# Kernel tuning notes

Measured on AMD Instinct MI355X. Metric: run time of the kernel, lower is better.

Reference implementation:

```python
import jax, jax.numpy as jnp
import numpy as np

WS = 8  # window size

def _rel_pos_index(ws):
    coords = np.stack(np.meshgrid(np.arange(ws), np.arange(ws), indexing='ij'))  # (2,ws,ws)
    cf = coords.reshape(2, -1)
    rel = (cf[:, :, None] - cf[:, None, :]).transpose(1, 2, 0).astype(np.int64)
    rel[..., 0] += ws - 1
    rel[..., 1] += ws - 1
    rel[..., 0] *= 2 * ws - 1
    return rel.sum(-1)  # (ws*ws, ws*ws)

REL_IDX = jnp.asarray(_rel_pos_index(WS).reshape(-1))

def _layernorm(x, g, b, eps=1e-5):
    m = x.mean(-1, keepdims=True)
    v = x.var(-1, keepdims=True)
    return (x - m) / jnp.sqrt(v + eps) * g + b

def setup_inputs() -> dict:
    key = jax.random.key(0)
    ks = jax.random.split(key, 32)
    B, Cw, Cs, H, W = 8, 64, 64, 128, 128
    dim, nH, hid = 256, 8, 1024
    n_bias = (2 * WS - 1) * (2 * WS - 1)
    s = 0.02
    d = {}
    d['LH'] = jax.random.normal(ks[0], (B, Cw, H, W), jnp.float32)
    d['HL'] = jax.random.normal(ks[1], (B, Cw, H, W), jnp.float32)
    d['HH'] = jax.random.normal(ks[2], (B, Cw, H, W), jnp.float32)
    d['Spat'] = jax.random.normal(ks[3], (B, Cs, H, W), jnp.float32)
    d['w_hllh'] = jax.random.normal(ks[4], (dim, 2 * Cw), jnp.float32) * s
    d['b_hllh'] = jnp.zeros((dim,), jnp.float32)
    d['w_hh'] = jax.random.normal(ks[5], (dim, Cw), jnp.float32) * s
    d['b_hh'] = jnp.zeros((dim,), jnp.float32)
    d['w_spat'] = jax.random.normal(ks[6], (dim, Cs), jnp.float32) * s
    d['b_spat'] = jnp.zeros((dim,), jnp.float32)
    d['ln1x_g'] = jnp.ones((dim,), jnp.float32)
    d['ln1x_b'] = jnp.zeros((dim,), jnp.float32)
    d['ln1y_g'] = jnp.ones((dim,), jnp.float32)
    d['ln1y_b'] = jnp.zeros((dim,), jnp.float32)
    d['qkv_w'] = jax.random.normal(ks[7], (dim, dim), jnp.float32) * s
    d['qkv_b'] = jnp.zeros((dim,), jnp.float32)
    d['qkv2_w'] = jax.random.normal(ks[8], (dim, dim), jnp.float32) * s
    d['qkv2_b'] = jnp.zeros((dim,), jnp.float32)
    d['qkv3_w'] = jax.random.normal(ks[9], (dim, dim), jnp.float32) * s
    d['qkv3_b'] = jnp.zeros((dim,), jnp.float32)
    d['proj_w'] = jax.random.normal(ks[10], (dim, dim), jnp.float32) * s
    d['proj_b'] = jnp.zeros((dim,), jnp.float32)
    d['rpb_table'] = jax.random.normal(ks[11], (n_bias, nH), jnp.float32) * s
    d['ln2_g'] = jnp.ones((dim,), jnp.float32)
    d['ln2_b'] = jnp.zeros((dim,), jnp.float32)
    d['fc1_w'] = jax.random.normal(ks[12], (hid, dim), jnp.float32) * s
    d['fc1_b'] = jnp.zeros((hid,), jnp.float32)
    d['fc2_w'] = jax.random.normal(ks[13], (dim, hid), jnp.float32) * s
    d['fc2_b'] = jnp.zeros((dim,), jnp.float32)
    return d

def _fwd(LH, HL, HH, Spat, w_hllh, b_hllh, w_hh, b_hh, w_spat, b_spat,
         ln1x_g, ln1x_b, ln1y_g, ln1y_b, qkv_w, qkv_b, qkv2_w, qkv2_b,
         qkv3_w, qkv3_b, proj_w, proj_b, rpb_table, ln2_g, ln2_b,
         fc1_w, fc1_b, fc2_w, fc2_b):
    B, _, H, W = LH.shape
    C = w_hllh.shape[0]
    nH = rpb_table.shape[1]
    hd = C // nH
    N = WS * WS
    # 1x1 convs to common dim, NHWC
    x = jnp.einsum('bchw,oc->bhwo', jnp.concatenate([LH, HL], axis=1), w_hllh) + b_hllh
    z0 = jnp.einsum('bchw,oc->bhwo', HH, w_hh) + b_hh
    y = jnp.einsum('bchw,oc->bhwo', Spat, w_spat) + b_spat
    shortcut = z0.reshape(B, H * W, C)
    xn = _layernorm(x, ln1x_g, ln1x_b)
    yn = _layernorm(y, ln1y_g, ln1y_b)
    # window partition (H,W divisible by WS)
    def part(t):
        t = t.reshape(B, H // WS, WS, W // WS, WS, C).transpose(0, 1, 3, 2, 4, 5)
        return t.reshape(-1, N, C)
    xw = part(xn)
    yw = part(yn)
    zw = yw  # original code: z = F.pad(y, ...) -> value stream is normalized y
    def heads(t, Wm, bm):
        return (t @ Wm.T + bm).reshape(-1, N, nH, hd).transpose(0, 2, 1, 3)
    q = heads(xw, qkv_w, qkv_b) * (hd ** -0.5)
    k = heads(yw, qkv2_w, qkv2_b)
    v = heads(zw, qkv3_w, qkv3_b)
    attn = jnp.einsum('bhnd,bhmd->bhnm', q, k)
    rpb = rpb_table[REL_IDX].reshape(N, N, nH).transpose(2, 0, 1)  # (nH,N,N)
    attn = jax.nn.softmax(attn + rpb[None], axis=-1)
    out = jnp.einsum('bhnm,bhmd->bnhd', attn, v).reshape(-1, N, C)
    out = out @ proj_w.T + proj_b
    # window reverse
    out = out.reshape(B, H // WS, W // WS, WS, WS, C).transpose(0, 1, 3, 2, 4, 5).reshape(B, H * W, C)
    zt = shortcut + out
    h = _layernorm(zt, ln2_g, ln2_b)
    h = jax.nn.gelu(h @ fc1_w.T + fc1_b, approximate=False) @ fc2_w.T + fc2_b
    zt = zt + h
    return zt.reshape(B, H, W, C).transpose(0, 3, 1, 2)

def reference(LH, HL, HH, Spat, w_hllh, b_hllh, w_hh, b_hh, w_spat, b_spat,
              ln1x_g, ln1x_b, ln1y_g, ln1y_b, qkv_w, qkv_b, qkv2_w, qkv2_b,
              qkv3_w, qkv3_b, proj_w, proj_b, rpb_table, ln2_g, ln2_b,
              fc1_w, fc1_b, fc2_w, fc2_b):
    return _fwd(LH, HL, HH, Spat, w_hllh, b_hllh, w_hh, b_hh, w_spat, b_spat,
                ln1x_g, ln1x_b, ln1y_g, ln1y_b, qkv_w, qkv_b, qkv2_w, qkv2_b,
                qkv3_w, qkv3_b, proj_w, proj_b, rpb_table, ln2_g, ln2_b,
                fc1_w, fc1_b, fc2_w, fc2_b)
```

## Files before the change

### kernel.cpp

```cpp
#include <hip/hip_runtime.h>
#include <math.h>

#define DI static __device__ __forceinline__

typedef __attribute__((ext_vector_type(8))) short bhalf8;
typedef __attribute__((ext_vector_type(4))) float floatx4;

DI unsigned short f2bf(float f){
  union { float f; unsigned u; } v; v.f = f;
  unsigned r = (v.u + 0x7fffu + ((v.u >> 16) & 1u)) >> 16;
  return (unsigned short)r;
}
DI float bflo(unsigned v){ return __uint_as_float(v << 16); }
DI float bfhi(unsigned v){ return __uint_as_float(v & 0xffff0000u); }
DI unsigned pk2(float a, float b){ return (unsigned)f2bf(a) | ((unsigned)f2bf(b) << 16); }
DI void unpack8(uint4 u, float* a){
  a[0]=bflo(u.x); a[1]=bfhi(u.x); a[2]=bflo(u.y); a[3]=bfhi(u.y);
  a[4]=bflo(u.z); a[5]=bfhi(u.z); a[6]=bflo(u.w); a[7]=bfhi(u.w);
}
DI float fc(float4 v, int j){ return j==0 ? v.x : (j==1 ? v.y : (j==2 ? v.z : v.w)); }
DI float gelu(float x){
  float u = x*(0.7978845608f + 0.0356774081f*x*x);
  float e = __expf(2.f*u);
  return x - x/(e + 1.f);
}

__global__ void k_scale_vec(const float* __restrict__ src, float* __restrict__ dst, int n, float s){
  int i = blockIdx.x*256 + threadIdx.x;
  if (i < n) dst[i] = src[i]*s;
}
__global__ void k_fragw(const float* __restrict__ src, unsigned short* __restrict__ dst,
                        int n, int K, float scale){
  int t = blockIdx.x*256 + threadIdx.x;
  if (t >= n) return;
  int j = t & 7, lane = (t >> 3) & 63, rest = t >> 9;
  int KS = K >> 5;
  int ks = rest % KS, nt = rest / KS;
  int row = nt*16 + (lane & 15);
  int col = ks*32 + ((lane >> 4) << 3) + j;
  dst[t] = f2bf(src[(size_t)row*K + col] * scale);
}
__global__ void k_bias(const float* __restrict__ rpb, float* __restrict__ biasf){
  int t = blockIdx.x*256 + threadIdx.x;
  int r = t & 3, lane = (t>>2) & 63, nt = (t>>8) & 3, mt = (t>>10) & 3, h = t>>12;
  int qtok = mt*16 + (lane>>4)*4 + r;
  int ktok = nt*16 + (lane & 15);
  int idx = ((qtok>>3) - (ktok>>3) + 7)*15 + ((qtok&7) - (ktok&7) + 7);
  biasf[t] = rpb[idx*8 + h];
}

__global__ __launch_bounds__(256) void k_front(
    const float* __restrict__ LH, const float* __restrict__ HL,
    const float* __restrict__ HH, const float* __restrict__ Sp,
    const unsigned short* __restrict__ wxf, const float* __restrict__ bx,
    const unsigned short* __restrict__ wzf, const float* __restrict__ bz,
    const unsigned short* __restrict__ wyf, const float* __restrict__ by,
    const float* __restrict__ g1x, const float* __restrict__ b1x,
    const float* __restrict__ g1y, const float* __restrict__ b1y,
    const unsigned short* __restrict__ wqf, const float* __restrict__ bq,
    const unsigned short* __restrict__ wkf, const float* __restrict__ bk,
    const unsigned short* __restrict__ wvf, const float* __restrict__ bv,
    unsigned short* __restrict__ z0, unsigned short* __restrict__ qg,
    unsigned short* __restrict__ kg, unsigned short* __restrict__ vtg)
{
  __shared__ __align__(16) unsigned short astg[64*72];
  __shared__ __align__(16) unsigned short sbufA[64*288];
  __shared__ __align__(16) unsigned short sbufB[64*264];
  float* part  = (float*)(sbufA + 16896);
  float* stats = part + 512;

  const int tid = threadIdx.x;
  const int lane = tid & 63, wave = tid >> 6, col = lane & 15, quad = lane >> 4;
  const int mB = blockIdx.x << 6;
  const int b  = mB >> 14;
  const int p0 = mB & 16383;
  const int hrow = p0 >> 7, w0 = p0 & 127;
  const int winb = b*256 + (hrow>>3)*16 + (w0>>3);
  const int tokrow = (hrow & 7)*8;
  const size_t pbase = (size_t)b * (64*16384) + p0;

  float4 f0, f1, f2, f3;
  auto stage_load = [&](const float* plane){
    const float* src = plane + (size_t)((tid>>4)*4)*16384 + (tid&15)*4;
    f0 = *(const float4*)(src);
    f1 = *(const float4*)(src + 16384);
    f2 = *(const float4*)(src + 32768);
    f3 = *(const float4*)(src + 49152);
  };
  auto stage_store = [&](){
    const int tq = tid & 15, c4 = (tid >> 4) * 4;
    #pragma unroll
    for (int j=0;j<4;++j){
      int tok = tq*4 + j;
      int kk = c4 ^ (((tok>>1)&7)<<3);
      uint2 u;
      u.x = pk2(fc(f0,j), fc(f1,j));
      u.y = pk2(fc(f2,j), fc(f3,j));
      *(uint2*)(astg + tok*72 + kk) = u;
    }
  };

  floatx4 c[4][4];
  auto zeroc = [&](){
    #pragma unroll
    for (int mt=0;mt<4;++mt)
      #pragma unroll
      for (int nt=0;nt<4;++nt) c[mt][nt] = (floatx4){0.f,0.f,0.f,0.f};
  };
  auto conv_step = [&](const unsigned short* wf, int KS, int ksg0){
    #pragma unroll
    for (int ksl=0; ksl<2; ++ksl){
      bhalf8 a[4];
      #pragma unroll
      for (int mt=0;mt<4;++mt){
        int tok = mt*16 + col;
        int kk = (ksl*32 + (quad<<3)) ^ (((tok>>1)&7)<<3);
        a[mt] = *(const bhalf8*)(astg + tok*72 + kk);
      }
      #pragma unroll
      for (int nt=0;nt<4;++nt){
        bhalf8 bfr = *(const bhalf8*)(wf + (size_t)(((wave*4+nt)*KS + ksg0 + ksl)*64 + lane)*8);
        #pragma unroll
        for (int mt=0;mt<4;++mt)
          c[mt][nt] = __builtin_amdgcn_mfma_f32_16x16x32_bf16(a[mt], bfr, c[mt][nt], 0, 0, 0);
      }
    }
  };
  auto ln_frag = [&](const float* bias, const float* g, const float* bb2, unsigned short* dst){
    float bv[4];
    #pragma unroll
    for (int nt=0;nt<4;++nt) bv[nt] = bias[wave*64 + nt*16 + col];
    #pragma unroll
    for (int mt=0;mt<4;++mt){
      #pragma unroll
      for (int r=0;r<4;++r){
        float s=0.f, q=0.f;
        #pragma unroll
        for (int nt=0;nt<4;++nt){
          float v = c[mt][nt][r] + bv[nt];
          c[mt][nt][r] = v; s += v; q += v*v;
        }
        s += __shfl_xor(s,1); q += __shfl_xor(q,1);
        s += __shfl_xor(s,2); q += __shfl_xor(q,2);
        s += __shfl_xor(s,4); q += __shfl_xor(q,4);
        s += __shfl_xor(s,8); q += __shfl_xor(q,8);
        if (col == 0){
          int tok = mt*16 + quad*4 + r;
          part[(wave*64+tok)*2+0] = s;
          part[(wave*64+tok)*2+1] = q;
        }
      }
    }
    __syncthreads();
    if (tid < 64){
      float s=0.f, q=0.f;
      #pragma unroll
      for (int w2=0;w2<4;++w2){ s += part[(w2*64+tid)*2]; q += part[(w2*64+tid)*2+1]; }
      float mean = s*(1.f/256.f);
      float var  = q*(1.f/256.f) - mean*mean;
      stats[tid*2]   = mean;
      stats[tid*2+1] = rsqrtf(var + 1e-5f);
    }
    __syncthreads();
    float gv[4], av[4];
    #pragma unroll
    for (int nt=0;nt<4;++nt){ int ch = wave*64+nt*16+col; gv[nt] = g[ch]; av[nt] = bb2[ch]; }
    #pragma unroll
    for (int mt=0;mt<4;++mt)
      #pragma unroll
      for (int r=0;r<4;++r){
        int tok = mt*16 + quad*4 + r;
        float mean = stats[tok*2], rstd = stats[tok*2+1];
        #pragma unroll
        for (int nt=0;nt<4;++nt)
          dst[tok*264 + wave*64 + nt*16 + col] = f2bf((c[mt][nt][r]-mean)*rstd*gv[nt] + av[nt]);
      }
    __syncthreads();
  };

  auto gemm = [&](const unsigned short* Abuf, const unsigned short* wf, const float* bias){
    #pragma unroll
    for (int mt=0;mt<4;++mt)
      #pragma unroll
      for (int nt=0;nt<4;++nt) c[mt][nt] = (floatx4){0.f,0.f,0.f,0.f};
    #pragma unroll
    for (int ks=0; ks<8; ++ks){
      bhalf8 a[4];
      #pragma unroll
      for (int mt=0;mt<4;++mt)
        a[mt] = *(const bhalf8*)(Abuf + (mt*16+col)*264 + ks*32 + (quad<<3));
      #pragma unroll
      for (int nt=0;nt<4;++nt){
        bhalf8 bf = *(const bhalf8*)(wf + (size_t)(((wave*4+nt)*8 + ks)*64 + lane)*8);
        #pragma unroll
        for (int mt=0;mt<4;++mt)
          c[mt][nt] = __builtin_amdgcn_mfma_f32_16x16x32_bf16(a[mt], bf, c[mt][nt], 0, 0, 0);
      }
    }
    #pragma unroll
    for (int nt=0;nt<4;++nt){
      float bb2 = bias[wave*64 + nt*16 + col];
      #pragma unroll
      for (int mt=0;mt<4;++mt)
        #pragma unroll
        for (int r=0;r<4;++r) c[mt][nt][r] += bb2;
    }
  };
  auto stage_write = [&](unsigned short* gout){
    __syncthreads();
    #pragma unroll
    for (int mt=0;mt<4;++mt)
      #pragma unroll
      for (int nt=0;nt<4;++nt)
        #pragma unroll
        for (int r=0;r<4;++r)
          sbufA[(mt*16+quad*4+r)*264 + wave*64 + nt*16 + col] = f2bf(c[mt][nt][r]);
    __syncthreads();
    int tok = tid >> 2, c0 = (tid & 3)*64;
    const uint4* s = (const uint4*)(sbufA + tok*264 + c0);
    uint4* d = (uint4*)(gout + ((size_t)(winb + (tok>>3)))*16384
                             + (size_t)(tokrow + (tok&7))*256 + c0);
    #pragma unroll
    for (int i=0;i<8;++i) d[i] = s[i];
  };

  stage_load(HH + pbase);
  stage_store();
  __syncthreads();
  stage_load(LH + pbase);
  zeroc(); conv_step(wzf, 2, 0);
  {
    #pragma unroll
    for (int nt=0;nt<4;++nt){
      float bzv = bz[wave*64 + nt*16 + col];
      #pragma unroll
      for (int mt=0;mt<4;++mt)
        #pragma unroll
        for (int r=0;r<4;++r) c[mt][nt][r] += bzv;
    }
  }
  stage_write(z0);
  stage_store();
  __syncthreads();
  stage_load(HL + pbase);
  zeroc(); conv_step(wxf, 4, 0);
  __syncthreads();
  stage_store();
  __syncthreads();
  stage_load(Sp + pbase);
  conv_step(wxf, 4, 2);
  __syncthreads();
  stage_store();
  ln_frag(bx, g1x, b1x, sbufA);
  zeroc(); conv_step(wyf, 2, 0);
  ln_frag(by, g1y, b1y, sbufB);
  gemm(sbufA, wqf, bq);
  stage_write(qg);
  gemm(sbufB, wkf, bk);
  stage_write(kg);
  gemm(sbufB, wvf, bv);
  __syncthreads();
  #pragma unroll
  for (int mt=0;mt<4;++mt)
    #pragma unroll
    for (int nt=0;nt<4;++nt){
      int ch = wave*64 + nt*16 + col;
      uint2 u; u.x = pk2(c[mt][nt][0], c[mt][nt][1]); u.y = pk2(c[mt][nt][2], c[mt][nt][3]);
      *(uint2*)(sbufA + ch*72 + mt*16 + quad*4) = u;
    }
  __syncthreads();
  {
    int ch = tid;
    #pragma unroll
    for (int wi=0; wi<8; ++wi){
      uint4 val = *(const uint4*)(sbufA + ch*72 + wi*8);
      *(uint4*)(vtg + ((size_t)(winb + wi))*16384 + ch*64 + tokrow) = val;
    }
  }
}

__global__ __launch_bounds__(256, 2) void k_attnproj(
    const unsigned short* __restrict__ qg, const unsigned short* kg,
    const unsigned short* vtg, const float* __restrict__ biasf,
    const unsigned short* __restrict__ wpf, const float* __restrict__ bp,
    const unsigned short* __restrict__ z0, unsigned short* kvz)
{
  __shared__ __align__(16) unsigned short Pb[4*64*72];
  __shared__ __align__(16) unsigned short Ob[64*264];
  const int tid = threadIdx.x, lane = tid & 63, wave = tid >> 6;
  const int col = lane & 15, quad = lane >> 4;
  const int win = blockIdx.x;
  const size_t wbase = (size_t)win * 16384;
  const unsigned short* qw = qg + wbase;
  const unsigned short* kw = kg + wbase;
  const unsigned short* vw = vtg + wbase;
  unsigned short* Pw = Pb + wave*64*72;

  #pragma unroll 1
  for (int hh=0; hh<2; ++hh){
    const int h = wave*2 + hh;
    bhalf8 qf[4], kf[4];
    #pragma unroll
    for (int mt=0;mt<4;++mt)
      qf[mt] = *(const bhalf8*)(qw + (mt*16+col)*256 + h*32 + (quad<<3));
    #pragma unroll
    for (int nt=0;nt<4;++nt)
      kf[nt] = *(const bhalf8*)(kw + (nt*16+col)*256 + h*32 + (quad<<3));
    floatx4 S[4][4];
    #pragma unroll
    for (int mt=0;mt<4;++mt)
      #pragma unroll
      for (int nt=0;nt<4;++nt) S[mt][nt] = (floatx4){0.f,0.f,0.f,0.f};
    #pragma unroll
    for (int mt=0;mt<4;++mt)
      #pragma unroll
      for (int nt=0;nt<4;++nt)
        S[mt][nt] = __builtin_amdgcn_mfma_f32_16x16x32_bf16(qf[mt], kf[nt], S[mt][nt], 0, 0, 0);
    #pragma unroll
    for (int mt=0;mt<4;++mt)
      #pragma unroll
      for (int nt=0;nt<4;++nt){
        float4 bb = *(const float4*)(biasf + (size_t)(((h*4+mt)*4+nt))*256 + lane*4);
        S[mt][nt][0] += bb.x; S[mt][nt][1] += bb.y; S[mt][nt][2] += bb.z; S[mt][nt][3] += bb.w;
      }
    float linv[4][4];
    #pragma unroll
    for (int mt=0;mt<4;++mt){
      #pragma unroll
      for (int r=0;r<4;++r){
        float mx = fmaxf(fmaxf(S[mt][0][r], S[mt][1][r]), fmaxf(S[mt][2][r], S[mt][3][r]));
        mx = fmaxf(mx, __shfl_xor(mx, 1));
        mx = fmaxf(mx, __shfl_xor(mx, 2));
        mx = fmaxf(mx, __shfl_xor(mx, 4));
        mx = fmaxf(mx, __shfl_xor(mx, 8));
        float e0 = __expf(S[mt][0][r]-mx), e1 = __expf(S[mt][1][r]-mx);
        float e2 = __expf(S[mt][2][r]-mx), e3 = __expf(S[mt][3][r]-mx);
        S[mt][0][r]=e0; S[mt][1][r]=e1; S[mt][2][r]=e2; S[mt][3][r]=e3;
        float l = e0+e1+e2+e3;
        l += __shfl_xor(l, 1);
        l += __shfl_xor(l, 2);
        l += __shfl_xor(l, 4);
        l += __shfl_xor(l, 8);
        linv[mt][r] = 1.f/l;
      }
    }
    #pragma unroll
    for (int mt=0;mt<4;++mt)
      #pragma unroll
      for (int nt=0;nt<4;++nt)
        #pragma unroll
        for (int r=0;r<4;++r)
          Pw[(mt*16+quad*4+r)*72 + nt*16 + col] = f2bf(S[mt][nt][r]);
    asm volatile("s_waitcnt lgkmcnt(0)" ::: "memory");
    floatx4 O[4][2];
    #pragma unroll
    for (int mt=0;mt<4;++mt){ O[mt][0]=(floatx4){0.f,0.f,0.f,0.f}; O[mt][1]=(floatx4){0.f,0.f,0.f,0.f}; }
    #pragma unroll
    for (int ks=0; ks<2; ++ks){
      bhalf8 vf[2];
      #pragma unroll
      for (int nt2=0;nt2<2;++nt2)
        vf[nt2] = *(const bhalf8*)(vw + (h*32 + nt2*16 + col)*64 + ks*32 + (quad<<3));
      #pragma unroll
      for (int mt=0;mt<4;++mt){
        bhalf8 pf = *(const bhalf8*)(Pw + (mt*16+col)*72 + ks*32 + (quad<<3));
        #pragma unroll
        for (int nt2=0;nt2<2;++nt2)
          O[mt][nt2] = __builtin_amdgcn_mfma_f32_16x16x32_bf16(pf, vf[nt2], O[mt][nt2], 0, 0, 0);
      }
    }
    #pragma unroll
    for (int mt=0;mt<4;++mt)
      #pragma unroll
      for (int nt2=0;nt2<2;++nt2)
        #pragma unroll
        for (int r=0;r<4;++r)
          Ob[(mt*16+quad*4+r)*264 + h*32 + nt2*16 + col] = f2bf(O[mt][nt2][r]*linv[mt][r]);
  }
  __syncthreads();

  floatx4 c[4][4];
  #pragma unroll
  for (int mt=0;mt<4;++mt)
    #pragma unroll
    for (int nt=0;nt<4;++nt) c[mt][nt] = (floatx4){0.f,0.f,0.f,0.f};
  #pragma unroll
  for (int ks=0; ks<8; ++ks){
    bhalf8 a[4];
    #pragma unroll
    for (int mt=0;mt<4;++mt)
      a[mt] = *(const bhalf8*)(Ob + (mt*16+col)*264 + ks*32 + (quad<<3));
    #pragma unroll
    for (int nt=0;nt<4;++nt){
      bhalf8 bf = *(const bhalf8*)(wpf + (size_t)(((wave*4+nt)*8 + ks)*64 + lane)*8);
      #pragma unroll
      for (int mt=0;mt<4;++mt)
        c[mt][nt] = __builtin_amdgcn_mfma_f32_16x16x32_bf16(a[mt], bf, c[mt][nt], 0, 0, 0);
    }
  }
  float bb[4];
  #pragma unroll
  for (int nt=0;nt<4;++nt) bb[nt] = bp[wave*64 + nt*16 + col];

  float* obuf = (float*)Pb;
  unsigned short* ztb = kvz + (size_t)win * 16384;
  #pragma unroll
  for (int p=0; p<2; ++p){
    __syncthreads();
    #pragma unroll
    for (int mt2=0;mt2<2;++mt2){
      int mt = p*2 + mt2;
      #pragma unroll
      for (int nt=0;nt<4;++nt)
        #pragma unroll
        for (int r=0;r<4;++r)
          obuf[(mt2*16+quad*4+r)*260 + wave*64 + nt*16 + col] = c[mt][nt][r] + bb[nt];
    }
    __syncthreads();
    {
      int tl = tid >> 3, c0 = (tid & 7)*32;
      int tok = p*32 + tl;
      const float4* s = (const float4*)(obuf + tl*260 + c0);
      const uint4* zp = (const uint4*)(z0 + ((size_t)win*64 + tok)*256 + c0);
      float zv[32];
      #pragma unroll
      for (int i=0;i<4;++i) unpack8(zp[i], zv + i*8);
      uint4* d = (uint4*)(ztb + (size_t)tok*256 + c0);
      #pragma unroll
      for (int i=0;i<4;++i){
        float4 a = s[2*i], b4 = s[2*i+1];
        float r0 = a.x  + zv[i*8+0], r1 = a.y  + zv[i*8+1];
        float r2 = a.z  + zv[i*8+2], r3 = a.w  + zv[i*8+3];
        float r4 = b4.x + zv[i*8+4], r5 = b4.y + zv[i*8+5];
        float r6 = b4.z + zv[i*8+6], r7 = b4.w + zv[i*8+7];
        uint4 u;
        u.x = pk2(r0,r1); u.y = pk2(r2,r3); u.z = pk2(r4,r5); u.w = pk2(r6,r7);
        d[i] = u;
      }
    }
  }
}

__global__ __launch_bounds__(256, 2) void k_mlp(
    const unsigned short* __restrict__ kvzt,
    const float* __restrict__ g2, const float* __restrict__ b2,
    const unsigned short* __restrict__ w1f, const float* __restrict__ fc1b,
    const unsigned short* __restrict__ w2f, const float* __restrict__ fc2b,
    float* __restrict__ out)
{
  __shared__ __align__(16) unsigned short smu[2*64*264];
  unsigned short* ztn  = smu;
  unsigned short* hbuf = smu + 64*264;
  float* ob = (float*)smu;

  const int tid  = threadIdx.x;
  const int mB   = blockIdx.x << 6;
  const int lane = tid & 63, wave = tid >> 6;
  const int col  = lane & 15, quad = lane >> 4;

  const int bb_ = mB >> 14;
  const int pp0 = mB & 16383;
  const int hrow = pp0 >> 7, w0 = pp0 & 127;
  const int winb = bb_*256 + (hrow>>3)*16 + (w0>>3);
  const int tokrow = (hrow & 7)*8;
  auto ztrow = [&](int tok)->size_t{
    return ((size_t)(winb + (tok>>3))*64 + (size_t)(tokrow + (tok&7))) * 256;
  };

  {
    const int tok = tid >> 2, qd = tid & 3;
    const uint4* zr = (const uint4*)(kvzt + ztrow(tok) + qd*64);
    float v[64];
    #pragma unroll
    for (int j=0;j<8;++j) unpack8(zr[j], v + j*8);
    float s=0.f, q=0.f;
    #pragma unroll
    for (int j=0;j<64;++j){ s += v[j]; q += v[j]*v[j]; }
    s += __shfl_xor(s,1); q += __shfl_xor(q,1);
    s += __shfl_xor(s,2); q += __shfl_xor(q,2);
    float mean = s*(1.f/256.f);
    float rstd = rsqrtf(q*(1.f/256.f) - mean*mean + 1e-5f);
    unsigned short* zd = ztn + tok*264 + qd*64;
    const float4* gp = (const float4*)(g2 + qd*64);
    const float4* bp = (const float4*)(b2 + qd*64);
    #pragma unroll
    for (int j8=0;j8<8;++j8){
      float4 g0 = gp[j8*2], g1 = gp[j8*2+1];
      float4 u0 = bp[j8*2], u1 = bp[j8*2+1];
      float r0 = (v[j8*8+0]-mean)*rstd*g0.x + u0.x;
      float r1 = (v[j8*8+1]-mean)*rstd*g0.y + u0.y;
      float r2 = (v[j8*8+2]-mean)*rstd*g0.z + u0.z;
      float r3 = (v[j8*8+3]-mean)*rstd*g0.w + u0.w;
      float r4 = (v[j8*8+4]-mean)*rstd*g1.x + u1.x;
      float r5 = (v[j8*8+5]-mean)*rstd*g1.y + u1.y;
      float r6 = (v[j8*8+6]-mean)*rstd*g1.z + u1.z;
      float r7 = (v[j8*8+7]-mean)*rstd*g1.w + u1.w;
      uint4 u;
      u.x=pk2(r0,r1); u.y=pk2(r2,r3); u.z=pk2(r4,r5); u.w=pk2(r6,r7);
      *(uint4*)(zd + j8*8) = u;
    }
  }
  __syncthreads();

  floatx4 oacc[4][4];
  #pragma unroll
  for (int i=0;i<4;++i)
    #pragma unroll
    for (int j=0;j<4;++j) oacc[i][j] = (floatx4){0.f,0.f,0.f,0.f};

  #pragma unroll 1
  for (int hb=0; hb<4; ++hb){
    float bv1[4];
    #pragma unroll
    for (int nt=0;nt<4;++nt) bv1[nt] = fc1b[hb*256 + wave*64 + nt*16 + col];
    #pragma unroll 1
    for (int mt=0; mt<4; ++mt){
      floatx4 hacc[4];
      #pragma unroll
      for (int nt=0;nt<4;++nt) hacc[nt] = (floatx4){0.f,0.f,0.f,0.f};
      #pragma unroll
      for (int ks=0; ks<8; ++ks){
        bhalf8 a = *(const bhalf8*)(ztn + (mt*16 + col)*264 + ks*32 + (quad<<3));
        #pragma unroll
        for (int nt=0; nt<4; ++nt){
          int gnt = hb*16 + wave*4 + nt;
          bhalf8 b = *(const bhalf8*)(w1f + (size_t)((gnt*8 + ks)*64 + lane)*8);
          hacc[nt] = __builtin_amdgcn_mfma_f32_16x16x32_bf16(a, b, hacc[nt], 0, 0, 0);
        }
      }
      #pragma unroll
      for (int nt=0; nt<4; ++nt){
        int ch = wave*64 + nt*16 + col;
        #pragma unroll
        for (int r=0;r<4;++r)
          hbuf[(mt*16 + quad*4 + r)*264 + ch] = f2bf(gelu(hacc[nt][r] + bv1[nt]));
      }
    }
    __syncthreads();
    #pragma unroll
    for (int mt=0; mt<4; ++mt){
      #pragma unroll
      for (int ks=0; ks<8; ++ks){
        bhalf8 a = *(const bhalf8*)(hbuf + (mt*16 + col)*264 + ks*32 + (quad<<3));
        #pragma unroll
        for (int ot=0; ot<4; ++ot){
          int go = wave*4 + ot;
          bhalf8 b = *(const bhalf8*)(w2f + (size_t)((go*32 + hb*8 + ks)*64 + lane)*8);
          oacc[mt][ot] = __builtin_amdgcn_mfma_f32_16x16x32_bf16(a, b, oacc[mt][ot], 0, 0, 0);
        }
      }
    }
    __syncthreads();
  }

  #pragma unroll
  for (int ot=0; ot<4; ++ot){
    int o = wave*64 + ot*16 + col;
    float bo = fc2b[o];
    #pragma unroll
    for (int mt=0; mt<4; ++mt){
      #pragma unroll
      for (int r=0;r<4;++r){
        int tok = mt*16 + quad*4 + r;
        float zv = bflo((unsigned)kvzt[ztrow(tok) + o]);
        ob[tok*257 + o] = oacc[mt][ot][r] + bo + zv;
      }
    }
  }
  __syncthreads();
  {
    const int b = mB >> 14, hw0 = mB & 16383;
    float* obase = out + (size_t)b*(256*16384) + hw0;
    #pragma unroll 1
    for (int it=0; it<64; ++it){
      int l = it*256 + tid;
      int o = l >> 6, tk = l & 63;
      obase[(size_t)o*16384 + tk] = ob[tk*257 + o];
    }
  }
}

extern "C" void kernel_launch(void* const* d_in, const int* in_sizes, int n_in,
                              void* d_out, int out_size, void* d_ws, size_t ws_size,
                              hipStream_t stream)
{
  (void)in_sizes; (void)n_in; (void)out_size; (void)ws_size;
  const float* LH    = (const float*)d_in[0];
  const float* HL    = (const float*)d_in[1];
  const float* HH    = (const float*)d_in[2];
  const float* Spat  = (const float*)d_in[3];
  const float* w_hllh= (const float*)d_in[4];
  const float* b_hllh= (const float*)d_in[5];
  const float* w_hh  = (const float*)d_in[6];
  const float* b_hh  = (const float*)d_in[7];
  const float* w_spat= (const float*)d_in[8];
  const float* b_spat= (const float*)d_in[9];
  const float* ln1x_g= (const float*)d_in[10];
  const float* ln1x_b= (const float*)d_in[11];
  const float* ln1y_g= (const float*)d_in[12];
  const float* ln1y_b= (const float*)d_in[13];
  const float* qkv_w = (const float*)d_in[14];
  const float* qkv_b = (const float*)d_in[15];
  const float* qkv2_w= (const float*)d_in[16];
  const float* qkv2_b= (const float*)d_in[17];
  const float* qkv3_w= (const float*)d_in[18];
  const float* qkv3_b= (const float*)d_in[19];
  const float* proj_w= (const float*)d_in[20];
  const float* proj_b= (const float*)d_in[21];
  const float* rpb   = (const float*)d_in[22];
  const float* ln2_g = (const float*)d_in[23];
  const float* ln2_b = (const float*)d_in[24];
  const float* fc1_w = (const float*)d_in[25];
  const float* fc1_b = (const float*)d_in[26];
  const float* fc2_w = (const float*)d_in[27];
  const float* fc2_b = (const float*)d_in[28];
  float* out = (float*)d_out;

  char* ws = (char*)d_ws;
  size_t off = 0;
  auto alloc = [&](size_t bytes)->void*{
    void* p = ws + off; off += (bytes + 255) & ~(size_t)255; return p;
  };
  const size_t M = 131072;
  unsigned short* z0  = (unsigned short*)alloc(M*256*2);
  unsigned short* qg  = (unsigned short*)alloc(M*256*2);
  char* kv_region     = (char*)alloc(M*256*4);
  unsigned short* kg  = (unsigned short*)kv_region;
  unsigned short* vtg = (unsigned short*)(kv_region + M*256*2);
  unsigned short* ztb = (unsigned short*)kv_region;
  unsigned short* wxf = (unsigned short*)alloc(256*128*2);
  unsigned short* wzf = (unsigned short*)alloc(256*64*2);
  unsigned short* wyf = (unsigned short*)alloc(256*64*2);
  unsigned short* wqf = (unsigned short*)alloc(256*256*2);
  unsigned short* wkf = (unsigned short*)alloc(256*256*2);
  unsigned short* wvf = (unsigned short*)alloc(256*256*2);
  unsigned short* wpf = (unsigned short*)alloc(256*256*2);
  unsigned short* w1f = (unsigned short*)alloc(1024*256*2);
  unsigned short* w2f = (unsigned short*)alloc(256*1024*2);
  float* biasf = (float*)alloc(32768*4);
  float* bqs = (float*)alloc(256*4);

  const float sc = 0.17677669529663687f;
  k_fragw<<<dim3(128),  dim3(256), 0, stream>>>(w_hllh, wxf, 256*128, 128, 1.f);
  k_fragw<<<dim3(64),   dim3(256), 0, stream>>>(w_hh,   wzf, 256*64,  64,  1.f);
  k_fragw<<<dim3(64),   dim3(256), 0, stream>>>(w_spat, wyf, 256*64,  64,  1.f);
  k_fragw<<<dim3(256),  dim3(256), 0, stream>>>(qkv_w,  wqf, 256*256, 256, sc);
  k_fragw<<<dim3(256),  dim3(256), 0, stream>>>(qkv2_w, wkf, 256*256, 256, 1.f);
  k_fragw<<<dim3(256),  dim3(256), 0, stream>>>(qkv3_w, wvf, 256*256, 256, 1.f);
  k_fragw<<<dim3(256),  dim3(256), 0, stream>>>(proj_w, wpf, 256*256, 256, 1.f);
  k_fragw<<<dim3(1024), dim3(256), 0, stream>>>(fc1_w,  w1f, 1024*256, 256, 1.f);
  k_fragw<<<dim3(1024), dim3(256), 0, stream>>>(fc2_w,  w2f, 256*1024, 1024, 1.f);
  k_bias <<<dim3(128),  dim3(256), 0, stream>>>(rpb, biasf);
  k_scale_vec<<<dim3(1), dim3(256), 0, stream>>>(qkv_b, bqs, 256, sc);

  k_front<<<dim3(2048), dim3(256), 0, stream>>>(LH, HL, HH, Spat,
      wxf, b_hllh, wzf, b_hh, wyf, b_spat,
      ln1x_g, ln1x_b, ln1y_g, ln1y_b,
      wqf, bqs, wkf, qkv2_b, wvf, qkv3_b,
      z0, qg, kg, vtg);
  k_attnproj<<<dim3(2048), dim3(256), 0, stream>>>(qg, kg, vtg, biasf, wpf, proj_b, z0, ztb);
  k_mlp<<<dim3(2048), dim3(256), 0, stream>>>(ztb, ln2_g, ln2_b,
      w1f, fc1_b, w2f, fc2_b, out);
}
```

Measured before the change: 810.4 us.

## Merge weight prep launches, reorder fragment layout, vectorize output stores

Eleven small preprocessing kernels are combined into one k_prep launch that dispatches on block index, which removes per-launch overhead. The weight fragment layout becomes lane-major with the k-step index innermost, so each lane's consecutive k-steps sit contiguously, and every GEMM's B-fragment addressing is updated to match. The final NCHW output store now writes float2 pairs, halving the store instruction count. The layout change could weaken coalescing across lanes within one load, since neighbouring lanes are now KS*16 bytes apart.

```diff
diff --git a/kernel.cpp b/kernel.cpp
--- a/kernel.cpp
+++ b/kernel.cpp
@@ -25,28 +25,62 @@
   return x - x/(e + 1.f);
 }
 
-__global__ void k_scale_vec(const float* __restrict__ src, float* __restrict__ dst, int n, float s){
-  int i = blockIdx.x*256 + threadIdx.x;
-  if (i < n) dst[i] = src[i]*s;
-}
-__global__ void k_fragw(const float* __restrict__ src, unsigned short* __restrict__ dst,
-                        int n, int K, float scale){
-  int t = blockIdx.x*256 + threadIdx.x;
-  if (t >= n) return;
-  int j = t & 7, lane = (t >> 3) & 63, rest = t >> 9;
-  int KS = K >> 5;
-  int ks = rest % KS, nt = rest / KS;
+DI void frag_pack(const float* __restrict__ src, unsigned short* __restrict__ dst,
+                  int t, int K, int ksbits, float scale){
+  int j = t & 7;
+  int ks = (t >> 3) & ((1<<ksbits)-1);
+  int lane = (t >> (3+ksbits)) & 63;
+  int nt = t >> (9+ksbits);
   int row = nt*16 + (lane & 15);
-  int col = ks*32 + ((lane >> 4) << 3) + j;
+  int col = (ks<<5) + ((lane >> 4) << 3) + j;
   dst[t] = f2bf(src[(size_t)row*K + col] * scale);
 }
-__global__ void k_bias(const float* __restrict__ rpb, float* __restrict__ biasf){
-  int t = blockIdx.x*256 + threadIdx.x;
-  int r = t & 3, lane = (t>>2) & 63, nt = (t>>8) & 3, mt = (t>>10) & 3, h = t>>12;
-  int qtok = mt*16 + (lane>>4)*4 + r;
-  int ktok = nt*16 + (lane & 15);
-  int idx = ((qtok>>3) - (ktok>>3) + 7)*15 + ((qtok&7) - (ktok&7) + 7);
-  biasf[t] = rpb[idx*8 + h];
+
+__global__ __launch_bounds__(256) void k_prep(
+    const float* __restrict__ w_hllh, const float* __restrict__ w_hh,
+    const float* __restrict__ w_spat, const float* __restrict__ qkv_w,
+    const float* __restrict__ qkv2_w, const float* __restrict__ qkv3_w,
+    const float* __restrict__ proj_w, const float* __restrict__ fc1_w,
+    const float* __restrict__ fc2_w, const float* __restrict__ rpb,
+    const float* __restrict__ qkv_b,
+    unsigned short* __restrict__ wxf, unsigned short* __restrict__ wzf,
+    unsigned short* __restrict__ wyf, unsigned short* __restrict__ wqf,
+    unsigned short* __restrict__ wkf, unsigned short* __restrict__ wvf,
+    unsigned short* __restrict__ wpf, unsigned short* __restrict__ w1f,
+    unsigned short* __restrict__ w2f, float* __restrict__ biasf,
+    float* __restrict__ bqs, float sc)
+{
+  int bid = blockIdx.x;
+  const int tid = threadIdx.x;
+  if (bid < 128){ frag_pack(w_hllh, wxf, bid*256+tid, 128, 2, 1.f); return; }
+  bid -= 128;
+  if (bid < 64){ frag_pack(w_hh, wzf, bid*256+tid, 64, 1, 1.f); return; }
+  bid -= 64;
+  if (bid < 64){ frag_pack(w_spat, wyf, bid*256+tid, 64, 1, 1.f); return; }
+  bid -= 64;
+  if (bid < 256){ frag_pack(qkv_w, wqf, bid*256+tid, 256, 3, sc); return; }
+  bid -= 256;
+  if (bid < 256){ frag_pack(qkv2_w, wkf, bid*256+tid, 256, 3, 1.f); return; }
+  bid -= 256;
+  if (bid < 256){ frag_pack(qkv3_w, wvf, bid*256+tid, 256, 3, 1.f); return; }
+  bid -= 256;
+  if (bid < 256){ frag_pack(proj_w, wpf, bid*256+tid, 256, 3, 1.f); return; }
+  bid -= 256;
+  if (bid < 1024){ frag_pack(fc1_w, w1f, bid*256+tid, 256, 3, 1.f); return; }
+  bid -= 1024;
+  if (bid < 1024){ frag_pack(fc2_w, w2f, bid*256+tid, 1024, 5, 1.f); return; }
+  bid -= 1024;
+  if (bid < 128){
+    int t = bid*256 + tid;
+    int r = t & 3, lane = (t>>2) & 63, nt = (t>>8) & 3, mt = (t>>10) & 3, h = t>>12;
+    int qtok = mt*16 + (lane>>4)*4 + r;
+    int ktok = nt*16 + (lane & 15);
+    int idx = ((qtok>>3) - (ktok>>3) + 7)*15 + ((qtok&7) - (ktok&7) + 7);
+    biasf[t] = rpb[idx*8 + h];
+    return;
+  }
+  bid -= 128;
+  if (bid == 0) bqs[tid] = qkv_b[tid]*sc;
 }
 
 __global__ __launch_bounds__(256) void k_front(
@@ -119,7 +153,7 @@
       }
       #pragma unroll
       for (int nt=0;nt<4;++nt){
-        bhalf8 bfr = *(const bhalf8*)(wf + (size_t)(((wave*4+nt)*KS + ksg0 + ksl)*64 + lane)*8);
+        bhalf8 bfr = *(const bhalf8*)(wf + (size_t)(((wave*4+nt)*64 + lane)*KS + ksg0 + ksl)*8);
         #pragma unroll
         for (int mt=0;mt<4;++mt)
           c[mt][nt] = __builtin_amdgcn_mfma_f32_16x16x32_bf16(a[mt], bfr, c[mt][nt], 0, 0, 0);
@@ -191,7 +225,7 @@
         a[mt] = *(const bhalf8*)(Abuf + (mt*16+col)*264 + ks*32 + (quad<<3));
       #pragma unroll
       for (int nt=0;nt<4;++nt){
-        bhalf8 bf = *(const bhalf8*)(wf + (size_t)(((wave*4+nt)*8 + ks)*64 + lane)*8);
+        bhalf8 bf = *(const bhalf8*)(wf + (size_t)(((wave*4+nt)*64 + lane)*8 + ks)*8);
         #pragma unroll
         for (int mt=0;mt<4;++mt)
           c[mt][nt] = __builtin_amdgcn_mfma_f32_16x16x32_bf16(a[mt], bf, c[mt][nt], 0, 0, 0);
@@ -392,7 +426,7 @@
       a[mt] = *(const bhalf8*)(Ob + (mt*16+col)*264 + ks*32 + (quad<<3));
     #pragma unroll
     for (int nt=0;nt<4;++nt){
-      bhalf8 bf = *(const bhalf8*)(wpf + (size_t)(((wave*4+nt)*8 + ks)*64 + lane)*8);
+      bhalf8 bf = *(const bhalf8*)(wpf + (size_t)(((wave*4+nt)*64 + lane)*8 + ks)*8);
       #pragma unroll
       for (int mt=0;mt<4;++mt)
         c[mt][nt] = __builtin_amdgcn_mfma_f32_16x16x32_bf16(a[mt], bf, c[mt][nt], 0, 0, 0);
@@ -524,7 +558,7 @@
         #pragma unroll
         for (int nt=0; nt<4; ++nt){
           int gnt = hb*16 + wave*4 + nt;
-          bhalf8 b = *(const bhalf8*)(w1f + (size_t)((gnt*8 + ks)*64 + lane)*8);
+          bhalf8 b = *(const bhalf8*)(w1f + (size_t)((gnt*64 + lane)*8 + ks)*8);
           hacc[nt] = __builtin_amdgcn_mfma_f32_16x16x32_bf16(a, b, hacc[nt], 0, 0, 0);
         }
       }
@@ -545,7 +579,7 @@
         #pragma unroll
         for (int ot=0; ot<4; ++ot){
           int go = wave*4 + ot;
-          bhalf8 b = *(const bhalf8*)(w2f + (size_t)((go*32 + hb*8 + ks)*64 + lane)*8);
+          bhalf8 b = *(const bhalf8*)(w2f + (size_t)((go*64 + lane)*32 + hb*8 + ks)*8);
           oacc[mt][ot] = __builtin_amdgcn_mfma_f32_16x16x32_bf16(a, b, oacc[mt][ot], 0, 0, 0);
         }
       }
@@ -572,10 +606,13 @@
     const int b = mB >> 14, hw0 = mB & 16383;
     float* obase = out + (size_t)b*(256*16384) + hw0;
     #pragma unroll 1
-    for (int it=0; it<64; ++it){
-      int l = it*256 + tid;
+    for (int it=0; it<32; ++it){
+      int l = it*512 + tid*2;
       int o = l >> 6, tk = l & 63;
-      obase[(size_t)o*16384 + tk] = ob[tk*257 + o];
+      float2 val;
+      val.x = ob[tk*257 + o];
+      val.y = ob[(tk+1)*257 + o];
+      *(float2*)(obase + (size_t)o*16384 + tk) = val;
     }
   }
 }
@@ -641,17 +678,10 @@
   float* bqs = (float*)alloc(256*4);
 
   const float sc = 0.17677669529663687f;
-  k_fragw<<<dim3(128),  dim3(256), 0, stream>>>(w_hllh, wxf, 256*128, 128, 1.f);
-  k_fragw<<<dim3(64),   dim3(256), 0, stream>>>(w_hh,   wzf, 256*64,  64,  1.f);
-  k_fragw<<<dim3(64),   dim3(256), 0, stream>>>(w_spat, wyf, 256*64,  64,  1.f);
-  k_fragw<<<dim3(256),  dim3(256), 0, stream>>>(qkv_w,  wqf, 256*256, 256, sc);
-  k_fragw<<<dim3(256),  dim3(256), 0, stream>>>(qkv2_w, wkf, 256*256, 256, 1.f);
-  k_fragw<<<dim3(256),  dim3(256), 0, stream>>>(qkv3_w, wvf, 256*256, 256, 1.f);
-  k_fragw<<<dim3(256),  dim3(256), 0, stream>>>(proj_w, wpf, 256*256, 256, 1.f);
-  k_fragw<<<dim3(1024), dim3(256), 0, stream>>>(fc1_w,  w1f, 1024*256, 256, 1.f);
-  k_fragw<<<dim3(1024), dim3(256), 0, stream>>>(fc2_w,  w2f, 256*1024, 1024, 1.f);
-  k_bias <<<dim3(128),  dim3(256), 0, stream>>>(rpb, biasf);
-  k_scale_vec<<<dim3(1), dim3(256), 0, stream>>>(qkv_b, bqs, 256, sc);
+  k_prep<<<dim3(3457), dim3(256), 0, stream>>>(
+      w_hllh, w_hh, w_spat, qkv_w, qkv2_w, qkv3_w, proj_w, fc1_w, fc2_w,
+      rpb, qkv_b,
+      wxf, wzf, wyf, wqf, wkf, wvf, wpf, w1f, w2f, biasf, bqs, sc);
 
   k_front<<<dim3(2048), dim3(256), 0, stream>>>(LH, HL, HH, Spat,
       wxf, b_hllh, wzf, b_hh, wyf, b_spat,
```

Result: slower. 1.278 ms (+57.7%).
